# Kernel tuning notes

Measured on AMD Instinct MI355X. Metric: run time of the kernel, lower is better.

## Reference

```python
import jax, jax.numpy as jnp
import numpy as np
import math

B, T, D = 2, 2048, 1024
H, DH = 16, 64          # num_heads, head_dim
DFF = 4096              # 4*d_model
EPS = 1e-5


def _layernorm(x, g, b):
    m = jnp.mean(x, axis=-1, keepdims=True)
    v = jnp.mean(jnp.square(x - m), axis=-1, keepdims=True)
    return (x - m) * jax.lax.rsqrt(v + EPS) * g + b


def setup_inputs() -> dict:
    key = jax.random.key(0)
    ks = jax.random.split(key, 6)
    s = 0.02
    return {
        "x": jax.random.normal(ks[0], (B, T, D), dtype=jnp.float32),
        "ln1_g": jnp.ones((D,), jnp.float32), "ln1_b": jnp.zeros((D,), jnp.float32),
        "ln2_g": jnp.ones((D,), jnp.float32), "ln2_b": jnp.zeros((D,), jnp.float32),
        "w_qkv": jax.random.normal(ks[1], (3 * D, D), jnp.float32) * s,
        "b_qkv": jnp.zeros((3 * D,), jnp.float32),
        "w_out": jax.random.normal(ks[2], (D, D), jnp.float32) * s,
        "b_out": jnp.zeros((D,), jnp.float32),
        "w1": jax.random.normal(ks[3], (DFF, D), jnp.float32) * s,
        "b1": jnp.zeros((DFF,), jnp.float32),
        "w2": jax.random.normal(ks[4], (D, DFF), jnp.float32) * s,
        "b2": jnp.zeros((D,), jnp.float32),
    }


def reference(x, ln1_g, ln1_b, ln2_g, ln2_b, w_qkv, b_qkv, w_out, b_out, w1, b1, w2, b2):
    # --- attention sublayer (Pre-LN) ---
    h = _layernorm(x, ln1_g, ln1_b)                       # [B,T,D]
    qkv = h @ w_qkv.T + b_qkv                             # [B,T,3D]
    qkv = qkv.reshape(B, T, 3, H, DH).transpose(2, 0, 3, 1, 4)  # [3,B,H,T,DH]
    q, k, v = qkv[0], qkv[1], qkv[2]
    scores = jnp.einsum('bhqd,bhkd->bhqk', q, k) / math.sqrt(DH)  # [B,H,T,T]
    causal = jnp.tril(jnp.ones((T, T), dtype=bool))
    scores = jnp.where(causal, scores, -jnp.inf)
    weights = jax.nn.softmax(scores, axis=-1)
    attn = jnp.einsum('bhqk,bhkd->bhqd', weights, v)      # [B,H,T,DH]
    attn = attn.transpose(0, 2, 1, 3).reshape(B, T, D)
    x = x + (attn @ w_out.T + b_out)

    # --- FFN sublayer (Pre-LN, exact GELU) ---
    h2 = _layernorm(x, ln2_g, ln2_b)
    ff = jax.nn.gelu(h2 @ w1.T + b1, approximate=False) @ w2.T + b2
    return x + ff
```

## Files before the change

### kernel.cpp

```cpp
#include <hip/hip_runtime.h>
#include <hip/hip_bf16.h>
#include <cmath>

typedef __bf16 bf16x8 __attribute__((ext_vector_type(8)));
typedef float  f32x4  __attribute__((ext_vector_type(4)));

#define LDS_AS __attribute__((address_space(3)))
#define GLB_AS __attribute__((address_space(1)))

__device__ __forceinline__ void gll16(const void* g, void* l) {
    __builtin_amdgcn_global_load_lds((const GLB_AS unsigned int*)g,
                                     (LDS_AS unsigned int*)l, 16, 0, 0);
}

__device__ __forceinline__ f32x4 mfma16(bf16x8 a, bf16x8 b, f32x4 c) {
    return __builtin_amdgcn_mfma_f32_16x16x32_bf16(a, b, c, 0, 0, 0);
}

__device__ __forceinline__ unsigned short f2bf(float f) {
    __hip_bfloat16 b = __float2bfloat16(f);
    return *reinterpret_cast<unsigned short*>(&b);
}

__device__ __forceinline__ bf16x8 swzfrag(const __hip_bfloat16* __restrict__ lds,
                                          int row, int cb)
{
    const int addr = row * 128 + (cb ^ ((row & 7) << 4));
    return *(const bf16x8*)((const char*)lds + addr);
}

__device__ __forceinline__ bf16x8 swzfrag32(const __hip_bfloat16* __restrict__ lds,
                                            int row, int cb)
{
    const int L = row >> 1;
    const int s = ((row & 1) << 2) | (cb >> 4);
    const int addr = (L << 7) | (((s ^ (L & 7)) << 4) | (cb & 15));
    return *(const bf16x8*)((const char*)lds + addr);
}

__device__ __forceinline__ void stage128x64B_swz(const char* __restrict__ base, int pitch,
                                                 char* __restrict__ lds, int t)
{
#pragma unroll
    for (int i = 0; i < 2; ++i) {
        const int d  = i * 4096 + t * 16;
        const int L  = d >> 7;
        const int sp = (d >> 4) & 7;
        const int s  = sp ^ (L & 7);
        const int r  = (L << 1) | (s >> 2);
        const int gx = (s & 3) << 4;
        gll16(base + (size_t)r * pitch + gx, lds + d);
    }
}

__device__ __forceinline__ void stage64x128B(const char* __restrict__ base, int pitch,
                                             char* __restrict__ lds, int t)
{
#pragma unroll
    for (int i = 0; i < 2; ++i) {
        const int d   = i * 4096 + t * 16;
        const int row = d >> 7;
        const int x   = d & 127;
        const int gx  = x ^ ((row & 7) << 4);
        gll16(base + (size_t)row * pitch + gx, lds + d);
    }
}

__device__ __forceinline__ void stage128x128B(const char* __restrict__ base, int pitch,
                                              char* __restrict__ lds, int t)
{
#pragma unroll
    for (int i = 0; i < 4; ++i) {
        const int d   = i * 4096 + t * 16;
        const int row = d >> 7;
        const int x   = d & 127;
        const int gx  = x ^ ((row & 7) << 4);
        gll16(base + (size_t)row * pitch + gx, lds + d);
    }
}

#define TB   2
#define TT   2048
#define TD   1024
#define TH   16
#define TDH  64
#define TDFF 4096
#define TM   4096

__global__ __launch_bounds__(256)
void cvt_kernel(const float* __restrict__ src, __hip_bfloat16* __restrict__ dst, int n4)
{
    int i = blockIdx.x * 256 + threadIdx.x;
    if (i >= n4) return;
    float4 v = ((const float4*)src)[i];
    ushort4 o;
    o.x = f2bf(v.x); o.y = f2bf(v.y); o.z = f2bf(v.z); o.w = f2bf(v.w);
    ((ushort4*)dst)[i] = o;
}

__global__ __launch_bounds__(256)
void ln_kernel(const float* __restrict__ x, const float* __restrict__ g,
               const float* __restrict__ b, __hip_bfloat16* __restrict__ out)
{
    const int row = blockIdx.x;
    const int t = threadIdx.x;
    const float4 v = *(const float4*)(x + (size_t)row * TD + t * 4);
    float s  = v.x + v.y + v.z + v.w;
    float ss = v.x*v.x + v.y*v.y + v.z*v.z + v.w*v.w;
#pragma unroll
    for (int d = 1; d < 64; d <<= 1) { s += __shfl_xor(s, d); ss += __shfl_xor(ss, d); }
    __shared__ float red[8];
    const int wv = t >> 6, lane = t & 63;
    if (lane == 0) { red[wv] = s; red[4 + wv] = ss; }
    __syncthreads();
    s  = red[0] + red[1] + red[2] + red[3];
    ss = red[4] + red[5] + red[6] + red[7];
    const float mean = s * (1.0f / TD);
    const float var  = ss * (1.0f / TD) - mean * mean;
    const float rstd = rsqrtf(var + 1e-5f);
    const float4 gv = *(const float4*)(g + t * 4);
    const float4 bv = *(const float4*)(b + t * 4);
    ushort4 o;
    o.x = f2bf((v.x - mean) * rstd * gv.x + bv.x);
    o.y = f2bf((v.y - mean) * rstd * gv.y + bv.y);
    o.z = f2bf((v.z - mean) * rstd * gv.z + bv.z);
    o.w = f2bf((v.w - mean) * rstd * gv.w + bv.w);
    *(ushort4*)(out + (size_t)row * TD + t * 4) = o;
}

template<int EPI>
__global__ __launch_bounds__(256)
void gemm_bt32(const __hip_bfloat16* __restrict__ A, const __hip_bfloat16* __restrict__ Bw,
               const float* __restrict__ bias,
               __hip_bfloat16* __restrict__ outb,
               __hip_bfloat16* __restrict__ qb, __hip_bfloat16* __restrict__ kb,
               __hip_bfloat16* __restrict__ vtb,
               int M, int N, int K)
{
    __shared__ __hip_bfloat16 ldsA[2][128 * 32];
    __shared__ __hip_bfloat16 ldsB[2][128 * 32];
    const int t = threadIdx.x;
    const int lane = t & 63, wv = t >> 6;
    const int wr = wv >> 1, wc = wv & 1;
    const int l15 = lane & 15, lg = lane >> 4;
    const int bn = blockIdx.x, bm = blockIdx.y;

    f32x4 acc[4][4] = {};

    const char* Ab = (const char*)(A  + (size_t)bm * 128 * K);
    const char* Bb = (const char*)(Bw + (size_t)bn * 128 * K);
    const int pitch = K * 2;

    const int nt = K >> 5;
    stage128x64B_swz(Ab, pitch, (char*)ldsA[0], t);
    stage128x64B_swz(Bb, pitch, (char*)ldsB[0], t);

    for (int it = 0; it < nt; ++it) {
        if (it + 1 < nt) {
            const size_t koff = (size_t)(it + 1) * 64;
            stage128x64B_swz(Ab + koff, pitch, (char*)ldsA[(it + 1) & 1], t);
            stage128x64B_swz(Bb + koff, pitch, (char*)ldsB[(it + 1) & 1], t);
            asm volatile("s_waitcnt vmcnt(4)" ::: "memory");
        } else {
            asm volatile("s_waitcnt vmcnt(0)" ::: "memory");
        }
        __builtin_amdgcn_s_barrier();
        __builtin_amdgcn_sched_barrier(0);
        const __hip_bfloat16* bufA = ldsA[it & 1];
        const __hip_bfloat16* bufB = ldsB[it & 1];
        bf16x8 af[4], bfr[4];
#pragma unroll
        for (int mf = 0; mf < 4; ++mf)
            af[mf] = swzfrag32(bufA, wr * 64 + mf * 16 + l15, lg * 16);
#pragma unroll
        for (int nf = 0; nf < 4; ++nf)
            bfr[nf] = swzfrag32(bufB, wc * 64 + nf * 16 + l15, lg * 16);
        __builtin_amdgcn_s_setprio(1);
#pragma unroll
        for (int mf = 0; mf < 4; ++mf)
#pragma unroll
            for (int nf = 0; nf < 4; ++nf)
                acc[mf][nf] = mfma16(af[mf], bfr[nf], acc[mf][nf]);
        __builtin_amdgcn_s_setprio(0);
        __builtin_amdgcn_s_barrier();
    }

#pragma unroll
    for (int mf = 0; mf < 4; ++mf) {
#pragma unroll
        for (int nf = 0; nf < 4; ++nf) {
#pragma unroll
            for (int r = 0; r < 4; ++r) {
                const int mg = bm * 128 + wr * 64 + mf * 16 + lg * 4 + r;
                const int ng = bn * 128 + wc * 64 + nf * 16 + l15;
                const float v = acc[mf][nf][r] + bias[ng];
                if constexpr (EPI == 2) {
                    const float ge = 0.5f * v * (1.0f + erff(v * 0.70710678118654752f));
                    outb[(size_t)mg * N + ng] = __float2bfloat16(ge);
                } else {
                    const int which = ng >> 10;
                    const int hh = (ng >> 6) & 15;
                    const int dh = ng & 63;
                    const int bb = mg >> 11;
                    const int tt2 = mg & 2047;
                    const int bhid = bb * TH + hh;
                    const __hip_bfloat16 bv = __float2bfloat16(v);
                    if (which == 0)      qb[((size_t)bhid * TT + tt2) * TDH + dh] = bv;
                    else if (which == 1) kb[((size_t)bhid * TT + tt2) * TDH + dh] = bv;
                    else                 vtb[((size_t)bhid * TDH + dh) * TT + tt2] = bv;
                }
            }
        }
    }
}

__global__ __launch_bounds__(512)
void gemm_sk(const __hip_bfloat16* __restrict__ A, const __hip_bfloat16* __restrict__ Bw,
             const float* __restrict__ bias, const float* __restrict__ resid,
             float* __restrict__ outf, int M, int N, int K)
{
    __shared__ char ldsraw[131072];
    const int t = threadIdx.x;
    const int tl = t & 255;
    const int lane = t & 63, w = t >> 6;
    const int grp = w >> 2;
    const int wl = w & 3;
    const int wr = wl >> 1, wc = wl & 1;
    const int l15 = lane & 15, lg = lane >> 4;
    const int bn = blockIdx.x, bm = blockIdx.y;

    f32x4 acc[4][4] = {};

    const int Kh = K >> 1;
    const char* Ab = (const char*)(A  + (size_t)bm * 128 * K) + (size_t)grp * Kh * 2;
    const char* Bb = (const char*)(Bw + (size_t)bn * 128 * K) + (size_t)grp * Kh * 2;
    const int pitch = K * 2;
    char* base = ldsraw + grp * 65536;

    const int nt = Kh >> 6;
    stage128x128B(Ab, pitch, base, tl);
    stage128x128B(Bb, pitch, base + 32768, tl);

    for (int it = 0; it < nt; ++it) {
        const int cb = (it & 1) * 16384;
        if (it + 1 < nt) {
            const size_t koff = (size_t)(it + 1) * 128;
            const int nb = ((it + 1) & 1) * 16384;
            stage128x128B(Ab + koff, pitch, base + nb, tl);
            stage128x128B(Bb + koff, pitch, base + 32768 + nb, tl);
            asm volatile("s_waitcnt vmcnt(8)" ::: "memory");
        } else {
            asm volatile("s_waitcnt vmcnt(0)" ::: "memory");
        }
        __builtin_amdgcn_s_barrier();
        __builtin_amdgcn_sched_barrier(0);
        const __hip_bfloat16* bufA = (const __hip_bfloat16*)(base + cb);
        const __hip_bfloat16* bufB = (const __hip_bfloat16*)(base + 32768 + cb);
        bf16x8 af[4][2], bfr[4][2];
#pragma unroll
        for (int mf = 0; mf < 4; ++mf)
#pragma unroll
            for (int kk = 0; kk < 2; ++kk)
                af[mf][kk] = swzfrag(bufA, wr * 64 + mf * 16 + l15, kk * 64 + lg * 16);
#pragma unroll
        for (int nf = 0; nf < 4; ++nf)
#pragma unroll
            for (int kk = 0; kk < 2; ++kk)
                bfr[nf][kk] = swzfrag(bufB, wc * 64 + nf * 16 + l15, kk * 64 + lg * 16);
        __builtin_amdgcn_s_setprio(1);
#pragma unroll
        for (int mf = 0; mf < 4; ++mf)
#pragma unroll
            for (int nf = 0; nf < 4; ++nf) {
                acc[mf][nf] = mfma16(af[mf][0], bfr[nf][0], acc[mf][nf]);
                acc[mf][nf] = mfma16(af[mf][1], bfr[nf][1], acc[mf][nf]);
            }
        __builtin_amdgcn_s_setprio(0);
        __builtin_amdgcn_s_barrier();
    }

    float* xch = (float*)ldsraw;
    if (grp == 1) {
#pragma unroll
        for (int mf = 0; mf < 4; ++mf)
#pragma unroll
            for (int nf = 0; nf < 4; ++nf)
#pragma unroll
                for (int r = 0; r < 4; ++r)
                    xch[(wr * 64 + mf * 16 + lg * 4 + r) * 132 + wc * 64 + nf * 16 + l15] =
                        acc[mf][nf][r];
    }
    __syncthreads();
    if (grp == 0) {
#pragma unroll
        for (int mf = 0; mf < 4; ++mf)
#pragma unroll
            for (int nf = 0; nf < 4; ++nf)
#pragma unroll
                for (int r = 0; r < 4; ++r) {
                    const int mgl = wr * 64 + mf * 16 + lg * 4 + r;
                    const int ngl = wc * 64 + nf * 16 + l15;
                    const int mg = bm * 128 + mgl;
                    const int ng = bn * 128 + ngl;
                    const size_t o = (size_t)mg * N + ng;
                    outf[o] = acc[mf][nf][r] + xch[mgl * 132 + ngl] + bias[ng] + resid[o];
                }
    }
}

__global__ __launch_bounds__(256)
void flash_kernel(const __hip_bfloat16* __restrict__ q, const __hip_bfloat16* __restrict__ k,
                  const __hip_bfloat16* __restrict__ vt, __hip_bfloat16* __restrict__ attn)
{
    const int L  = blockIdx.y * gridDim.x + blockIdx.x;
    const int cu = L & 255;
    const int s  = L >> 8;
    const int q0 = cu & 31;
    const int qt = (s & 1) ? (31 - q0) : q0;
    const int bh = s * 8 + (cu >> 5);

    const int t = threadIdx.x;
    const int w = t >> 6, lane = t & 63;
    const int l15 = lane & 15, lg = lane >> 4;
    const int qrow0 = qt * 64 + w * 16;
    const __hip_bfloat16* Qb = q  + (size_t)bh * TT * TDH;
    const __hip_bfloat16* Kb = k  + (size_t)bh * TT * TDH;
    const __hip_bfloat16* Vb = vt + (size_t)bh * TDH * TT;

    __shared__ __hip_bfloat16 kt[2][64 * 64];
    __shared__ __hip_bfloat16 vtt[2][64 * 64];
    __shared__ __hip_bfloat16 plds[4][16 * 64];

    bf16x8 qa[2];
#pragma unroll
    for (int c = 0; c < 2; ++c)
        qa[c] = *(const bf16x8*)(Qb + (size_t)(qrow0 + l15) * TDH + c * 32 + lg * 8);

    f32x4 o[4] = {};
    float mrun = -INFINITY, lrun = 0.0f;

    const int nt = qt + 1;
    int cur = 0;
    stage64x128B((const char*)Kb, 128, (char*)kt[0], t);
    stage64x128B((const char*)Vb, TT * 2, (char*)vtt[0], t);
    __syncthreads();

    for (int it = 0; it < nt; ++it) {
        const int kv0 = it * 64;
        if (it + 1 < nt) {
            stage64x128B((const char*)Kb + (size_t)(kv0 + 64) * 128, 128, (char*)kt[cur ^ 1], t);
            stage64x128B((const char*)Vb + (size_t)(kv0 + 64) * 2, TT * 2, (char*)vtt[cur ^ 1], t);
        }
        f32x4 sc[4] = {};
        __builtin_amdgcn_s_setprio(1);
#pragma unroll
        for (int j = 0; j < 4; ++j) {
            const bf16x8 kb0 = swzfrag(kt[cur], j * 16 + l15, lg * 16);
            const bf16x8 kb1 = swzfrag(kt[cur], j * 16 + l15, 64 + lg * 16);
            sc[j] = mfma16(kb0, qa[0], sc[j]);
            sc[j] = mfma16(kb1, qa[1], sc[j]);
        }
        __builtin_amdgcn_s_setprio(0);
        if (it == nt - 1) {
            const int qg = qrow0 + l15;
#pragma unroll
            for (int j = 0; j < 4; ++j)
#pragma unroll
                for (int r = 0; r < 4; ++r) {
                    const int kvg = kv0 + j * 16 + lg * 4 + r;
                    sc[j][r] = (kvg <= qg) ? sc[j][r] * 0.125f : -INFINITY;
                }
        } else {
#pragma unroll
            for (int j = 0; j < 4; ++j)
#pragma unroll
                for (int r = 0; r < 4; ++r) sc[j][r] *= 0.125f;
        }
        float pm;
        {
            float m0 = fmaxf(fmaxf(sc[0][0], sc[0][1]), fmaxf(sc[0][2], sc[0][3]));
            float m1 = fmaxf(fmaxf(sc[1][0], sc[1][1]), fmaxf(sc[1][2], sc[1][3]));
            float m2 = fmaxf(fmaxf(sc[2][0], sc[2][1]), fmaxf(sc[2][2], sc[2][3]));
            float m3 = fmaxf(fmaxf(sc[3][0], sc[3][1]), fmaxf(sc[3][2], sc[3][3]));
            pm = fmaxf(fmaxf(m0, m1), fmaxf(m2, m3));
        }
        pm = fmaxf(pm, __shfl_xor(pm, 16));
        pm = fmaxf(pm, __shfl_xor(pm, 32));

        const float mn = fmaxf(mrun, pm);
        const float alpha = __expf(mrun - mn);
        mrun = mn;
        f32x4 p[4];
        float rs = 0.0f;
#pragma unroll
        for (int j = 0; j < 4; ++j) {
            float a = 0.0f;
#pragma unroll
            for (int r = 0; r < 4; ++r) { p[j][r] = __expf(sc[j][r] - mn); a += p[j][r]; }
            rs += a;
        }
        rs += __shfl_xor(rs, 16);
        rs += __shfl_xor(rs, 32);
        lrun = lrun * alpha + rs;
#pragma unroll
        for (int nf = 0; nf < 4; ++nf)
#pragma unroll
            for (int r = 0; r < 4; ++r) o[nf][r] *= alpha;
        {
            __hip_bfloat16* pw = plds[w];
#pragma unroll
            for (int j = 0; j < 4; ++j) {
                ushort4 pk;
                pk.x = f2bf(p[j][0]); pk.y = f2bf(p[j][1]);
                pk.z = f2bf(p[j][2]); pk.w = f2bf(p[j][3]);
                const int cb = j * 32 + lg * 8;
                *(ushort4*)((char*)pw + l15 * 128 + (cb ^ ((l15 & 7) << 4))) = pk;
            }
        }
        asm volatile("s_waitcnt lgkmcnt(0)" ::: "memory");
        __builtin_amdgcn_sched_barrier(0);
        bf16x8 pb[2];
#pragma unroll
        for (int c = 0; c < 2; ++c)
            pb[c] = swzfrag(plds[w], l15, c * 64 + lg * 16);
        __builtin_amdgcn_s_setprio(1);
#pragma unroll
        for (int nf = 0; nf < 4; ++nf) {
            const bf16x8 vb0 = swzfrag(vtt[cur], nf * 16 + l15, lg * 16);
            const bf16x8 vb1 = swzfrag(vtt[cur], nf * 16 + l15, 64 + lg * 16);
            o[nf] = mfma16(vb0, pb[0], o[nf]);
            o[nf] = mfma16(vb1, pb[1], o[nf]);
        }
        __builtin_amdgcn_s_setprio(0);
        __syncthreads();
        cur ^= 1;
    }

    const int bb = bh >> 4, hh = bh & 15;
    const float inv = 1.0f / lrun;
    const int tt = qrow0 + l15;
#pragma unroll
    for (int nf = 0; nf < 4; ++nf) {
        const int d0 = nf * 16 + lg * 4;
        ushort4 st;
        st.x = f2bf(o[nf][0] * inv);
        st.y = f2bf(o[nf][1] * inv);
        st.z = f2bf(o[nf][2] * inv);
        st.w = f2bf(o[nf][3] * inv);
        *(ushort4*)(attn + ((size_t)(bb * TT + tt)) * TD + hh * TDH + d0) = st;
    }
}

extern "C" void kernel_launch(void* const* d_in, const int* in_sizes, int n_in,
                              void* d_out, int out_size, void* d_ws, size_t ws_size,
                              hipStream_t stream)
{
    const float* x     = (const float*)d_in[0];
    const float* ln1_g = (const float*)d_in[1];
    const float* ln1_b = (const float*)d_in[2];
    const float* ln2_g = (const float*)d_in[3];
    const float* ln2_b = (const float*)d_in[4];
    const float* w_qkv = (const float*)d_in[5];
    const float* b_qkv = (const float*)d_in[6];
    const float* w_out = (const float*)d_in[7];
    const float* b_out = (const float*)d_in[8];
    const float* w1    = (const float*)d_in[9];
    const float* b1    = (const float*)d_in[10];
    const float* w2    = (const float*)d_in[11];
    const float* b2    = (const float*)d_in[12];

    char* ws = (char*)d_ws;
    __hip_bfloat16* wqkv_bf = (__hip_bfloat16*)(ws + 0);
    __hip_bfloat16* wout_bf = (__hip_bfloat16*)(ws + 6291456);
    __hip_bfloat16* w1_bf   = (__hip_bfloat16*)(ws + 8388608);
    __hip_bfloat16* w2_bf   = (__hip_bfloat16*)(ws + 16777216);
    float*          x2      = (float*)(ws + 25165824);
    __hip_bfloat16* hbuf    = (__hip_bfloat16*)(ws + 41943040);
    __hip_bfloat16* qbuf    = (__hip_bfloat16*)(ws + 50331648);
    __hip_bfloat16* kbuf    = (__hip_bfloat16*)(ws + 58720256);
    __hip_bfloat16* vtbuf   = (__hip_bfloat16*)(ws + 67108864);
    __hip_bfloat16* attnbuf = (__hip_bfloat16*)(ws + 75497472);
    __hip_bfloat16* ff1     = (__hip_bfloat16*)(ws + 50331648);

    cvt_kernel<<<3072, 256, 0, stream>>>(w_qkv, wqkv_bf, 3 * TD * TD / 4);
    cvt_kernel<<<1024, 256, 0, stream>>>(w_out, wout_bf, TD * TD / 4);
    cvt_kernel<<<4096, 256, 0, stream>>>(w1, w1_bf, TDFF * TD / 4);
    cvt_kernel<<<4096, 256, 0, stream>>>(w2, w2_bf, TD * TDFF / 4);

    ln_kernel<<<TM, 256, 0, stream>>>(x, ln1_g, ln1_b, hbuf);
    gemm_bt32<0><<<dim3(24, 32), 256, 0, stream>>>(hbuf, wqkv_bf, b_qkv,
                                                   nullptr, qbuf, kbuf, vtbuf,
                                                   TM, 3 * TD, TD);
    flash_kernel<<<dim3(32, 32), 256, 0, stream>>>(qbuf, kbuf, vtbuf, attnbuf);
    gemm_sk<<<dim3(8, 32), 512, 0, stream>>>(attnbuf, wout_bf, b_out, x,
                                             x2, TM, TD, TD);
    ln_kernel<<<TM, 256, 0, stream>>>(x2, ln2_g, ln2_b, hbuf);
    gemm_bt32<2><<<dim3(32, 32), 256, 0, stream>>>(hbuf, w1_bf, b1,
                                                   ff1, nullptr, nullptr, nullptr,
                                                   TM, TDFF, TD);
    gemm_sk<<<dim3(8, 32), 512, 0, stream>>>(ff1, w2_bf, b2, x2,
                                             (float*)d_out, TM, TD, TDFF);
}
```

Measured before the change: 248.9 us.

## Enlarge flash attention query tile, fuse weight conversions, drop GEMM setprio

The flash kernel now handles 128 query rows per block, with each wave owning 32 rows as two 16-row groups. Each K/V fragment read from LDS is therefore reused for twice the MFMAs, and the grid is halved. The four weight-conversion launches are merged into one kernel that picks its source by index range, cutting launch overhead. The s_setprio hints around the MFMA loops in both GEMM kernels are removed. The flash change raises register and LDS use per block and lowers block count, which may hurt occupancy and load balance.

```diff
diff --git a/kernel.cpp b/kernel.cpp
--- a/kernel.cpp
+++ b/kernel.cpp
@@ -88,14 +88,22 @@
 #define TM   4096
 
 __global__ __launch_bounds__(256)
-void cvt_kernel(const float* __restrict__ src, __hip_bfloat16* __restrict__ dst, int n4)
-{
-    int i = blockIdx.x * 256 + threadIdx.x;
-    if (i >= n4) return;
-    float4 v = ((const float4*)src)[i];
+void cvt4_kernel(const float* __restrict__ s0, const float* __restrict__ s1,
+                 const float* __restrict__ s2, const float* __restrict__ s3,
+                 __hip_bfloat16* __restrict__ d0, __hip_bfloat16* __restrict__ d1,
+                 __hip_bfloat16* __restrict__ d2, __hip_bfloat16* __restrict__ d3)
+{
+    const int i = blockIdx.x * 256 + threadIdx.x;
+    const float* src; __hip_bfloat16* dst; int off;
+    if (i < 786432)       { src = s0; dst = d0; off = 0; }
+    else if (i < 1048576) { src = s1; dst = d1; off = 786432; }
+    else if (i < 2097152) { src = s2; dst = d2; off = 1048576; }
+    else                  { src = s3; dst = d3; off = 2097152; }
+    const int j = i - off;
+    float4 v = ((const float4*)src)[j];
     ushort4 o;
     o.x = f2bf(v.x); o.y = f2bf(v.y); o.z = f2bf(v.z); o.w = f2bf(v.w);
-    ((ushort4*)dst)[i] = o;
+    ((ushort4*)dst)[j] = o;
 }
 
 __global__ __launch_bounds__(256)
@@ -175,13 +183,11 @@
 #pragma unroll
         for (int nf = 0; nf < 4; ++nf)
             bfr[nf] = swzfrag32(bufB, wc * 64 + nf * 16 + l15, lg * 16);
-        __builtin_amdgcn_s_setprio(1);
 #pragma unroll
         for (int mf = 0; mf < 4; ++mf)
 #pragma unroll
             for (int nf = 0; nf < 4; ++nf)
                 acc[mf][nf] = mfma16(af[mf], bfr[nf], acc[mf][nf]);
-        __builtin_amdgcn_s_setprio(0);
         __builtin_amdgcn_s_barrier();
     }
 
@@ -267,7 +273,6 @@
 #pragma unroll
             for (int kk = 0; kk < 2; ++kk)
                 bfr[nf][kk] = swzfrag(bufB, wc * 64 + nf * 16 + l15, kk * 64 + lg * 16);
-        __builtin_amdgcn_s_setprio(1);
 #pragma unroll
         for (int mf = 0; mf < 4; ++mf)
 #pragma unroll
@@ -275,7 +280,6 @@
                 acc[mf][nf] = mfma16(af[mf][0], bfr[nf][0], acc[mf][nf]);
                 acc[mf][nf] = mfma16(af[mf][1], bfr[nf][1], acc[mf][nf]);
             }
-        __builtin_amdgcn_s_setprio(0);
         __builtin_amdgcn_s_barrier();
     }
 
@@ -315,31 +319,36 @@
     const int L  = blockIdx.y * gridDim.x + blockIdx.x;
     const int cu = L & 255;
     const int s  = L >> 8;
-    const int q0 = cu & 31;
-    const int qt = (s & 1) ? (31 - q0) : q0;
-    const int bh = s * 8 + (cu >> 5);
+    const int q0 = cu & 15;
+    const int qt = s ? (15 - q0) : q0;
+    const int bh = s * 16 + (cu >> 4);
 
     const int t = threadIdx.x;
     const int w = t >> 6, lane = t & 63;
     const int l15 = lane & 15, lg = lane >> 4;
-    const int qrow0 = qt * 64 + w * 16;
+    const int qrow0 = qt * 128 + w * 32;
     const __hip_bfloat16* Qb = q  + (size_t)bh * TT * TDH;
     const __hip_bfloat16* Kb = k  + (size_t)bh * TT * TDH;
     const __hip_bfloat16* Vb = vt + (size_t)bh * TDH * TT;
 
     __shared__ __hip_bfloat16 kt[2][64 * 64];
     __shared__ __hip_bfloat16 vtt[2][64 * 64];
-    __shared__ __hip_bfloat16 plds[4][16 * 64];
-
-    bf16x8 qa[2];
-#pragma unroll
-    for (int c = 0; c < 2; ++c)
-        qa[c] = *(const bf16x8*)(Qb + (size_t)(qrow0 + l15) * TDH + c * 32 + lg * 8);
-
-    f32x4 o[4] = {};
-    float mrun = -INFINITY, lrun = 0.0f;
-
-    const int nt = qt + 1;
+    __shared__ __hip_bfloat16 plds[4][32 * 64];
+
+    bf16x8 qa[2][2];
+#pragma unroll
+    for (int g = 0; g < 2; ++g)
+#pragma unroll
+        for (int c = 0; c < 2; ++c)
+            qa[g][c] = *(const bf16x8*)(Qb + (size_t)(qrow0 + g * 16 + l15) * TDH
+                                        + c * 32 + lg * 8);
+
+    f32x4 o[2][4] = {};
+    float mrun[2], lrun[2];
+#pragma unroll
+    for (int g = 0; g < 2; ++g) { mrun[g] = -INFINITY; lrun[g] = 0.0f; }
+
+    const int nt = 2 * qt + 2;
     int cur = 0;
     stage64x128B((const char*)Kb, 128, (char*)kt[0], t);
     stage64x128B((const char*)Vb, TT * 2, (char*)vtt[0], t);
@@ -351,85 +360,100 @@
             stage64x128B((const char*)Kb + (size_t)(kv0 + 64) * 128, 128, (char*)kt[cur ^ 1], t);
             stage64x128B((const char*)Vb + (size_t)(kv0 + 64) * 2, TT * 2, (char*)vtt[cur ^ 1], t);
         }
-        f32x4 sc[4] = {};
+        f32x4 sc[2][4] = {};
         __builtin_amdgcn_s_setprio(1);
 #pragma unroll
         for (int j = 0; j < 4; ++j) {
             const bf16x8 kb0 = swzfrag(kt[cur], j * 16 + l15, lg * 16);
             const bf16x8 kb1 = swzfrag(kt[cur], j * 16 + l15, 64 + lg * 16);
-            sc[j] = mfma16(kb0, qa[0], sc[j]);
-            sc[j] = mfma16(kb1, qa[1], sc[j]);
+            sc[0][j] = mfma16(kb0, qa[0][0], sc[0][j]);
+            sc[0][j] = mfma16(kb1, qa[0][1], sc[0][j]);
+            sc[1][j] = mfma16(kb0, qa[1][0], sc[1][j]);
+            sc[1][j] = mfma16(kb1, qa[1][1], sc[1][j]);
         }
         __builtin_amdgcn_s_setprio(0);
-        if (it == nt - 1) {
-            const int qg = qrow0 + l15;
-#pragma unroll
-            for (int j = 0; j < 4; ++j)
-#pragma unroll
-                for (int r = 0; r < 4; ++r) {
-                    const int kvg = kv0 + j * 16 + lg * 4 + r;
-                    sc[j][r] = (kvg <= qg) ? sc[j][r] * 0.125f : -INFINITY;
+        if (it >= nt - 2) {
+#pragma unroll
+            for (int g = 0; g < 2; ++g) {
+                const int qg = qrow0 + g * 16 + l15;
+#pragma unroll
+                for (int j = 0; j < 4; ++j)
+#pragma unroll
+                    for (int r = 0; r < 4; ++r) {
+                        const int kvg = kv0 + j * 16 + lg * 4 + r;
+                        sc[g][j][r] = (kvg <= qg) ? sc[g][j][r] * 0.125f : -INFINITY;
+                    }
+            }
+        } else {
+#pragma unroll
+            for (int g = 0; g < 2; ++g)
+#pragma unroll
+                for (int j = 0; j < 4; ++j)
+#pragma unroll
+                    for (int r = 0; r < 4; ++r) sc[g][j][r] *= 0.125f;
+        }
+#pragma unroll
+        for (int g = 0; g < 2; ++g) {
+            float pm;
+            {
+                float m0 = fmaxf(fmaxf(sc[g][0][0], sc[g][0][1]), fmaxf(sc[g][0][2], sc[g][0][3]));
+                float m1 = fmaxf(fmaxf(sc[g][1][0], sc[g][1][1]), fmaxf(sc[g][1][2], sc[g][1][3]));
+                float m2 = fmaxf(fmaxf(sc[g][2][0], sc[g][2][1]), fmaxf(sc[g][2][2], sc[g][2][3]));
+                float m3 = fmaxf(fmaxf(sc[g][3][0], sc[g][3][1]), fmaxf(sc[g][3][2], sc[g][3][3]));
+                pm = fmaxf(fmaxf(m0, m1), fmaxf(m2, m3));
+            }
+            pm = fmaxf(pm, __shfl_xor(pm, 16));
+            pm = fmaxf(pm, __shfl_xor(pm, 32));
+
+            const float mn = fmaxf(mrun[g], pm);
+            const float alpha = __expf(mrun[g] - mn);
+            mrun[g] = mn;
+            f32x4 p[4];
+            float rs = 0.0f;
+#pragma unroll
+            for (int j = 0; j < 4; ++j) {
+                float a = 0.0f;
+#pragma unroll
+                for (int r = 0; r < 4; ++r) { p[j][r] = __expf(sc[g][j][r] - mn); a += p[j][r]; }
+                rs += a;
+            }
+            rs += __shfl_xor(rs, 16);
+            rs += __shfl_xor(rs, 32);
+            lrun[g] = lrun[g] * alpha + rs;
+#pragma unroll
+            for (int nf = 0; nf < 4; ++nf)
+#pragma unroll
+                for (int r = 0; r < 4; ++r) o[g][nf][r] *= alpha;
+            {
+                __hip_bfloat16* pw = plds[w];
+                const int prow = g * 16 + l15;
+#pragma unroll
+                for (int j = 0; j < 4; ++j) {
+                    ushort4 pk;
+                    pk.x = f2bf(p[j][0]); pk.y = f2bf(p[j][1]);
+                    pk.z = f2bf(p[j][2]); pk.w = f2bf(p[j][3]);
+                    const int cb = j * 32 + lg * 8;
+                    *(ushort4*)((char*)pw + prow * 128 + (cb ^ ((prow & 7) << 4))) = pk;
                 }
-        } else {
-#pragma unroll
-            for (int j = 0; j < 4; ++j)
-#pragma unroll
-                for (int r = 0; r < 4; ++r) sc[j][r] *= 0.125f;
-        }
-        float pm;
-        {
-            float m0 = fmaxf(fmaxf(sc[0][0], sc[0][1]), fmaxf(sc[0][2], sc[0][3]));
-            float m1 = fmaxf(fmaxf(sc[1][0], sc[1][1]), fmaxf(sc[1][2], sc[1][3]));
-            float m2 = fmaxf(fmaxf(sc[2][0], sc[2][1]), fmaxf(sc[2][2], sc[2][3]));
-            float m3 = fmaxf(fmaxf(sc[3][0], sc[3][1]), fmaxf(sc[3][2], sc[3][3]));
-            pm = fmaxf(fmaxf(m0, m1), fmaxf(m2, m3));
-        }
-        pm = fmaxf(pm, __shfl_xor(pm, 16));
-        pm = fmaxf(pm, __shfl_xor(pm, 32));
-
-        const float mn = fmaxf(mrun, pm);
-        const float alpha = __expf(mrun - mn);
-        mrun = mn;
-        f32x4 p[4];
-        float rs = 0.0f;
-#pragma unroll
-        for (int j = 0; j < 4; ++j) {
-            float a = 0.0f;
-#pragma unroll
-            for (int r = 0; r < 4; ++r) { p[j][r] = __expf(sc[j][r] - mn); a += p[j][r]; }
-            rs += a;
-        }
-        rs += __shfl_xor(rs, 16);
-        rs += __shfl_xor(rs, 32);
-        lrun = lrun * alpha + rs;
-#pragma unroll
-        for (int nf = 0; nf < 4; ++nf)
-#pragma unroll
-            for (int r = 0; r < 4; ++r) o[nf][r] *= alpha;
-        {
-            __hip_bfloat16* pw = plds[w];
-#pragma unroll
-            for (int j = 0; j < 4; ++j) {
-                ushort4 pk;
-                pk.x = f2bf(p[j][0]); pk.y = f2bf(p[j][1]);
-                pk.z = f2bf(p[j][2]); pk.w = f2bf(p[j][3]);
-                const int cb = j * 32 + lg * 8;
-                *(ushort4*)((char*)pw + l15 * 128 + (cb ^ ((l15 & 7) << 4))) = pk;
             }
         }
         asm volatile("s_waitcnt lgkmcnt(0)" ::: "memory");
         __builtin_amdgcn_sched_barrier(0);
-        bf16x8 pb[2];
-#pragma unroll
-        for (int c = 0; c < 2; ++c)
-            pb[c] = swzfrag(plds[w], l15, c * 64 + lg * 16);
+        bf16x8 pb[2][2];
+#pragma unroll
+        for (int g = 0; g < 2; ++g)
+#pragma unroll
+            for (int c = 0; c < 2; ++c)
+                pb[g][c] = swzfrag(plds[w], g * 16 + l15, c * 64 + lg * 16);
         __builtin_amdgcn_s_setprio(1);
 #pragma unroll
         for (int nf = 0; nf < 4; ++nf) {
             const bf16x8 vb0 = swzfrag(vtt[cur], nf * 16 + l15, lg * 16);
             const bf16x8 vb1 = swzfrag(vtt[cur], nf * 16 + l15, 64 + lg * 16);
-            o[nf] = mfma16(vb0, pb[0], o[nf]);
-            o[nf] = mfma16(vb1, pb[1], o[nf]);
+            o[0][nf] = mfma16(vb0, pb[0][0], o[0][nf]);
+            o[0][nf] = mfma16(vb1, pb[0][1], o[0][nf]);
+            o[1][nf] = mfma16(vb0, pb[1][0], o[1][nf]);
+            o[1][nf] = mfma16(vb1, pb[1][1], o[1][nf]);
         }
         __builtin_amdgcn_s_setprio(0);
         __syncthreads();
@@ -437,17 +461,20 @@
     }
 
     const int bb = bh >> 4, hh = bh & 15;
-    const float inv = 1.0f / lrun;
-    const int tt = qrow0 + l15;
-#pragma unroll
-    for (int nf = 0; nf < 4; ++nf) {
-        const int d0 = nf * 16 + lg * 4;
-        ushort4 st;
-        st.x = f2bf(o[nf][0] * inv);
-        st.y = f2bf(o[nf][1] * inv);
-        st.z = f2bf(o[nf][2] * inv);
-        st.w = f2bf(o[nf][3] * inv);
-        *(ushort4*)(attn + ((size_t)(bb * TT + tt)) * TD + hh * TDH + d0) = st;
+#pragma unroll
+    for (int g = 0; g < 2; ++g) {
+        const float inv = 1.0f / lrun[g];
+        const int tt = qrow0 + g * 16 + l15;
+#pragma unroll
+        for (int nf = 0; nf < 4; ++nf) {
+            const int d0 = nf * 16 + lg * 4;
+            ushort4 st;
+            st.x = f2bf(o[g][nf][0] * inv);
+            st.y = f2bf(o[g][nf][1] * inv);
+            st.z = f2bf(o[g][nf][2] * inv);
+            st.w = f2bf(o[g][nf][3] * inv);
+            *(ushort4*)(attn + ((size_t)(bb * TT + tt)) * TD + hh * TDH + d0) = st;
+        }
     }
 }
 
@@ -482,16 +509,14 @@
     __hip_bfloat16* attnbuf = (__hip_bfloat16*)(ws + 75497472);
     __hip_bfloat16* ff1     = (__hip_bfloat16*)(ws + 50331648);
 
-    cvt_kernel<<<3072, 256, 0, stream>>>(w_qkv, wqkv_bf, 3 * TD * TD / 4);
-    cvt_kernel<<<1024, 256, 0, stream>>>(w_out, wout_bf, TD * TD / 4);
-    cvt_kernel<<<4096, 256, 0, stream>>>(w1, w1_bf, TDFF * TD / 4);
-    cvt_kernel<<<4096, 256, 0, stream>>>(w2, w2_bf, TD * TDFF / 4);
+    cvt4_kernel<<<12288, 256, 0, stream>>>(w_qkv, w_out, w1, w2,
+                                           wqkv_bf, wout_bf, w1_bf, w2_bf);
 
     ln_kernel<<<TM, 256, 0, stream>>>(x, ln1_g, ln1_b, hbuf);
     gemm_bt32<0><<<dim3(24, 32), 256, 0, stream>>>(hbuf, wqkv_bf, b_qkv,
                                                    nullptr, qbuf, kbuf, vtbuf,
                                                    TM, 3 * TD, TD);
-    flash_kernel<<<dim3(32, 32), 256, 0, stream>>>(qbuf, kbuf, vtbuf, attnbuf);
+    flash_kernel<<<dim3(16, 32), 256, 0, stream>>>(qbuf, kbuf, vtbuf, attnbuf);
     gemm_sk<<<dim3(8, 32), 512, 0, stream>>>(attnbuf, wout_bf, b_out, x,
                                              x2, TM, TD, TD);
     ln_kernel<<<TM, 256, 0, stream>>>(x2, ln2_g, ln2_b, hbuf);
```

Measured after the change: 249.5 us. No clear change (+0.2%).
